# Optimization experiments

Measured on AMD Instinct MI355X. Metric: run time of the kernel, lower is better.

Reference implementation:

```python
import jax, jax.numpy as jnp
import numpy as np

NUM_EMBEDDINGS = 1024
EMBEDDING_DIM = 64
COMMITMENT_COST = 0.25


def setup_inputs() -> dict:
    key = jax.random.key(0)
    k1, k2 = jax.random.split(key)
    inputs = jax.random.normal(k1, (16, EMBEDDING_DIM, 64, 64), dtype=jnp.float32)
    # nn.Embedding weight init: uniform(-1/K, 1/K)
    emb = jax.random.uniform(
        k2, (NUM_EMBEDDINGS, EMBEDDING_DIM), dtype=jnp.float32,
        minval=-1.0 / NUM_EMBEDDINGS, maxval=1.0 / NUM_EMBEDDINGS)
    return {"inputs": inputs, "emb": emb}


def reference(inputs, emb):
    # NCHW -> NHWC
    x = jnp.transpose(inputs, (0, 2, 3, 1))  # [B,H,W,D]
    B, H, W, D = x.shape
    K = emb.shape[0]
    flat = x.reshape(-1, D)  # [N,D]

    # squared L2 distances to every codebook entry: [N,K]
    distances = (jnp.sum(flat * flat, axis=1, keepdims=True)
                 + jnp.sum(emb * emb, axis=1)
                 - 2.0 * jnp.matmul(flat, emb.T))
    idx = jnp.argmin(distances, axis=1)  # [N]
    indices = idx.reshape(B, H, W)[:, None]  # [B,1,H,W]

    # gather == one-hot @ emb, but without the dense matmul
    quantized = emb[idx].reshape(B, H, W, D)

    e_latent_loss = jnp.mean((jax.lax.stop_gradient(quantized) - x) ** 2)
    q_latent_loss = jnp.mean((quantized - jax.lax.stop_gradient(x)) ** 2)
    loss = q_latent_loss + COMMITMENT_COST * e_latent_loss

    # straight-through estimator
    quantized_st = x + jax.lax.stop_gradient(quantized - x)

    # one-hot encodings are part of the module's return contract
    encodings = jax.nn.one_hot(idx, K, dtype=jnp.float32)  # [N,K]
    avg_probs = jnp.mean(encodings, axis=0)
    perplexity = jnp.exp(-jnp.sum(avg_probs * jnp.log(avg_probs + 1e-10)))

    quantized_out = jnp.transpose(quantized_st, (0, 3, 1, 2))  # back to NCHW
    return (loss, quantized_out, perplexity, encodings, indices)
```

## Files before the change

kernel.cpp:

```cpp
#include <hip/hip_runtime.h>

#define NPIX    65536
#define D       64
#define KCODES  1024
#define PIXB    64
#define BLOCK   512
#define XPAD    68
#define XBPAD   72
#define CAP     64
#define GFAC    0.036f

#define QUANT_OFF 1
#define PERP_OFF  4194305
#define ENC_OFF   4194306u
#define IDX_OFF   71303170u


typedef float f32x4 __attribute__((ext_vector_type(4)));
typedef short bf16x8 __attribute__((ext_vector_type(8)));

__device__ __forceinline__ unsigned short f2bf(float f) {
    unsigned u = __float_as_uint(f);
    return (unsigned short)((u + 0x7fffu + ((u >> 16) & 1u)) >> 16);
}

__global__ __launch_bounds__(256) void vq_init(const float* __restrict__ emb,
                                               double* __restrict__ loss_sum,
                                               int* __restrict__ counts,
                                               float* __restrict__ se,
                                               unsigned short* __restrict__ ebf) {
    int t = blockIdx.x * 256 + threadIdx.x;
    if (t == 0) *loss_sum = 0.0;
    if (t < KCODES) {
        counts[t] = 0;
        const float* e = emb + (size_t)t * D;
        float r[8];
        #pragma unroll
        for (int j = 0; j < 8; ++j) r[j] = __fmul_rn(e[j], e[j]);
        #pragma unroll
        for (int i = 8; i < D; i += 8)
            #pragma unroll
            for (int j = 0; j < 8; ++j)
                r[j] = __fadd_rn(r[j], __fmul_rn(e[i + j], e[i + j]));
        float X = __fadd_rn(__fadd_rn(r[0], r[1]), __fadd_rn(r[2], r[3]));
        float Y = __fadd_rn(__fadd_rn(r[4], r[5]), __fadd_rn(r[6], r[7]));
        se[t] = __fadd_rn(X, Y);
        #pragma unroll
        for (int j = 0; j < D; ++j) ebf[(t << 6) + j] = f2bf(e[j]);
    }
}

__global__ __launch_bounds__(512) void vq_main(const float* __restrict__ in,
                                               const float* __restrict__ emb,
                                               const float* __restrict__ se,
                                               const unsigned short* __restrict__ ebf,
                                               float* __restrict__ out,
                                               double* __restrict__ loss_sum,
                                               int* __restrict__ counts) {
    __shared__ float xs[PIXB][XPAD];
    __shared__ unsigned short xb[PIXB][XBPAD];
    __shared__ float sls[KCODES];
    __shared__ float wmin[8][PIXB];
    __shared__ float gate[PIXB];
    __shared__ float sxs[PIXB];
    __shared__ float smx[PIXB];
    __shared__ float semaxsq;
    __shared__ int   cnt[PIXB];
    __shared__ unsigned short list[PIXB][CAP];
    __shared__ int   skfin[PIXB];

    const int tid  = threadIdx.x;
    const int lane = tid & 63;
    const int wid  = tid >> 6;
    const int n0   = blockIdx.x * PIXB;
    const int b    = n0 >> 12;
    const int s0   = n0 & 4095;

    {
        const float* base = in + ((size_t)b << 18) + s0;
        #pragma unroll
        for (int i = 0; i < 8; ++i) {
            int d = wid + (i << 3);
            float v = base[((size_t)d << 12) + lane];
            xs[lane][d] = v;
            xb[lane][d] = f2bf(v);
        }
        sls[tid] = se[tid];
        sls[tid + 512] = se[tid + 512];
    }
    __syncthreads();

    if (tid < PIXB) {
        float r[8];
        #pragma unroll
        for (int j = 0; j < 8; ++j) {
            float v = xs[tid][j];
            r[j] = __fmul_rn(v, v);
        }
        #pragma unroll
        for (int i = 8; i < D; i += 8)
            #pragma unroll
            for (int j = 0; j < 8; ++j) {
                float v = xs[tid][i + j];
                r[j] = __fadd_rn(r[j], __fmul_rn(v, v));
            }
        float X = __fadd_rn(__fadd_rn(r[0], r[1]), __fadd_rn(r[2], r[3]));
        float Y = __fadd_rn(__fadd_rn(r[4], r[5]), __fadd_rn(r[6], r[7]));
        sxs[tid] = __fadd_rn(X, Y);
        float mx = sls[tid << 4];
        #pragma unroll
        for (int j = 1; j < 16; ++j) mx = fmaxf(mx, sls[(tid << 4) + j]);
        smx[tid] = mx;
    }

    const int wbase = wid * 128;
    const int arow  = lane & 15;
    const int kgrp  = (lane >> 4) << 3;
    const int rbase = (lane >> 4) << 2;

    bf16x8 af[2][4];
    #pragma unroll
    for (int ks = 0; ks < 2; ++ks)
        #pragma unroll
        for (int pt = 0; pt < 4; ++pt)
            af[ks][pt] = *(const bf16x8*)&xb[pt * 16 + arow][ks * 32 + kgrp];

    float mreg[4][4];
    #pragma unroll
    for (int pt = 0; pt < 4; ++pt)
        #pragma unroll
        for (int r = 0; r < 4; ++r) mreg[pt][r] = 3.0e38f;

    #pragma unroll
    for (int s = 0; s < 2; ++s) {
        const int cbase = wbase + s * 64;
        f32x4 acc[4][4];
        #pragma unroll
        for (int pt = 0; pt < 4; ++pt)
            #pragma unroll
            for (int kt = 0; kt < 4; ++kt) acc[pt][kt] = (f32x4){0.f, 0.f, 0.f, 0.f};
        #pragma unroll
        for (int ks = 0; ks < 2; ++ks) {
            #pragma unroll
            for (int kt = 0; kt < 4; ++kt) {
                int code = cbase + kt * 16 + arow;
                bf16x8 bf_ = *(const bf16x8*)(ebf + ((size_t)code << 6) + ks * 32 + kgrp);
                #pragma unroll
                for (int pt = 0; pt < 4; ++pt)
                    acc[pt][kt] = __builtin_amdgcn_mfma_f32_16x16x32_bf16(
                        af[ks][pt], bf_, acc[pt][kt], 0, 0, 0);
            }
        }
        #pragma unroll
        for (int pt = 0; pt < 4; ++pt)
            #pragma unroll
            for (int kt = 0; kt < 4; ++kt) {
                int code = cbase + kt * 16 + arow;
                #pragma unroll
                for (int r = 0; r < 4; ++r) {
                    float sv = __fsub_rn(sls[code], __fmul_rn(2.0f, acc[pt][kt][r]));
                    mreg[pt][r] = fminf(mreg[pt][r], sv);
                }
            }
    }
    #pragma unroll
    for (int m = 1; m < 16; m <<= 1)
        #pragma unroll
        for (int pt = 0; pt < 4; ++pt)
            #pragma unroll
            for (int r = 0; r < 4; ++r)
                mreg[pt][r] = fminf(mreg[pt][r], __shfl_xor(mreg[pt][r], m));
    if (arow == 0) {
        #pragma unroll
        for (int pt = 0; pt < 4; ++pt)
            #pragma unroll
            for (int r = 0; r < 4; ++r)
                wmin[wid][pt * 16 + rbase + r] = mreg[pt][r];
    }
    __syncthreads();

    if (tid == 0) {
        float mx = smx[0];
        #pragma unroll
        for (int j = 1; j < PIXB; ++j) mx = fmaxf(mx, smx[j]);
        semaxsq = mx;
    }
    __syncthreads();

    if (tid < PIXB) {
        float gm = wmin[0][tid];
        #pragma unroll
        for (int w = 1; w < 8; ++w) gm = fminf(gm, wmin[w][tid]);
        gate[tid] = gm + GFAC * sqrtf(sxs[tid] * semaxsq);
        cnt[tid] = 0;
    }
    __syncthreads();

    #pragma unroll
    for (int s = 0; s < 2; ++s) {
        const int cbase = wbase + s * 64;
        f32x4 acc[4][4];
        #pragma unroll
        for (int pt = 0; pt < 4; ++pt)
            #pragma unroll
            for (int kt = 0; kt < 4; ++kt) acc[pt][kt] = (f32x4){0.f, 0.f, 0.f, 0.f};
        #pragma unroll
        for (int ks = 0; ks < 2; ++ks) {
            #pragma unroll
            for (int kt = 0; kt < 4; ++kt) {
                int code = cbase + kt * 16 + arow;
                bf16x8 bf_ = *(const bf16x8*)(ebf + ((size_t)code << 6) + ks * 32 + kgrp);
                #pragma unroll
                for (int pt = 0; pt < 4; ++pt)
                    acc[pt][kt] = __builtin_amdgcn_mfma_f32_16x16x32_bf16(
                        af[ks][pt], bf_, acc[pt][kt], 0, 0, 0);
            }
        }
        #pragma unroll
        for (int pt = 0; pt < 4; ++pt)
            #pragma unroll
            for (int kt = 0; kt < 4; ++kt) {
                int code = cbase + kt * 16 + arow;
                #pragma unroll
                for (int r = 0; r < 4; ++r) {
                    float sv = __fsub_rn(sls[code], __fmul_rn(2.0f, acc[pt][kt][r]));
                    int px = pt * 16 + rbase + r;
                    if (sv <= gate[px]) {
                        int slot = atomicAdd(&cnt[px], 1);
                        if (slot < CAP) list[px][slot] = (unsigned short)code;
                    }
                }
            }
    }
    __syncthreads();

    {
        const int px = tid >> 3, c0 = tid & 7;
        const int cn = cnt[px];
        float bv = 3.0e38f;
        int   bk = 0x7fffffff;
        if (cn > CAP) {
            for (int k = c0; k < KCODES; k += 8) {
                const float* er = emb + ((size_t)k << 6);
                float m = 0.f;
                #pragma unroll
                for (int d = 0; d < D; ++d) m = fmaf(xs[px][d], er[d], m);
                float sv = __fsub_rn(__fadd_rn(sxs[px], sls[k]), __fmul_rn(2.0f, m));
                if (sv < bv || (sv == bv && k < bk)) { bv = sv; bk = k; }
            }
        } else {
            for (int i = c0; i < cn; i += 8) {
                int k = list[px][i];
                const float* er = emb + ((size_t)k << 6);
                float m = 0.f;
                #pragma unroll
                for (int d = 0; d < D; ++d) m = fmaf(xs[px][d], er[d], m);
                float sv = __fsub_rn(__fadd_rn(sxs[px], sls[k]), __fmul_rn(2.0f, m));
                if (sv < bv || (sv == bv && k < bk)) { bv = sv; bk = k; }
            }
        }
        #pragma unroll
        for (int m = 4; m; m >>= 1) {
            float ov = __shfl_xor(bv, m);
            int   ok = __shfl_xor(bk, m);
            if (ov < bv || (ov == bv && ok < bk)) { bv = ov; bk = ok; }
        }
        if (c0 == 0) {
            skfin[px] = bk;
            atomicAdd(&counts[bk], 1);
            out[IDX_OFF + (unsigned)(n0 + px)] = (float)bk;
        }
    }
    __syncthreads();

    {
        float* qbase = out + QUANT_OFF + ((size_t)b << 18) + s0;
        float mse = 0.f;
        #pragma unroll
        for (int i = 0; i < 8; ++i) {
            int d = (wid << 3) + i;
            float q = emb[((size_t)skfin[lane] << 6) + d];
            qbase[((size_t)d << 12) + lane] = q;
            float df = q - xs[lane][d];
            mse = fmaf(df, df, mse);
        }
        #pragma unroll
        for (int off = 32; off; off >>= 1) mse += __shfl_down(mse, off);
        if (lane == 0) atomicAdd(loss_sum, (double)mse);
    }

    float4* dst4 = (float4*)(out + ENC_OFF + (size_t)n0 * KCODES + 2);
    for (int i = tid; i < 16383; i += BLOCK) {
        int flat = (i << 2) + 2;
        int r0 = flat >> 10;
        int r1 = (flat + 3) >> 10;
        int k0 = skfin[r0];
        int k1 = skfin[r1];
        int c  = flat & 1023;
        float4 v;
        v.x = (c == k0) ? 1.f : 0.f;
        v.y = (c + 1 == k0) ? 1.f : 0.f;
        v.z = (((flat + 2) & 1023) == k1) ? 1.f : 0.f;
        v.w = (((flat + 3) & 1023) == k1) ? 1.f : 0.f;
        dst4[i] = v;
    }
    if (tid == 0) {
        float2* dh = (float2*)(out + ENC_OFF + (size_t)n0 * KCODES);
        int kh = skfin[0];
        float2 h2; h2.x = (kh == 0) ? 1.f : 0.f; h2.y = (kh == 1) ? 1.f : 0.f;
        *dh = h2;
        float2* dt = (float2*)(out + ENC_OFF + (size_t)n0 * KCODES + 65534);
        int kt = skfin[63];
        float2 t2; t2.x = (kt == 1022) ? 1.f : 0.f; t2.y = (kt == 1023) ? 1.f : 0.f;
        *dt = t2;
    }
}

__global__ __launch_bounds__(256) void vq_fin(const double* __restrict__ loss_sum,
                                              const int* __restrict__ counts,
                                              float* __restrict__ out) {
    __shared__ double red[256];
    int t = threadIdx.x;
    double ent = 0.0;
    for (int k = t; k < KCODES; k += 256) {
        double p = (double)counts[k] / 65536.0;
        ent -= p * log(p + 1e-10);
    }
    red[t] = ent;
    __syncthreads();
    for (int o = 128; o; o >>= 1) {
        if (t < o) red[t] += red[t + o];
        __syncthreads();
    }
    if (t == 0) {
        out[PERP_OFF] = (float)exp(red[0]);
        out[0] = (float)(1.25 * (*loss_sum) / 4194304.0);
    }
}

extern "C" void kernel_launch(void* const* d_in, const int* in_sizes, int n_in,
                              void* d_out, int out_size, void* d_ws, size_t ws_size,
                              hipStream_t stream) {
    const float* in  = (const float*)d_in[0];
    const float* emb = (const float*)d_in[1];
    float* out = (float*)d_out;

    double*         loss_sum = (double*)d_ws;
    int*            counts   = (int*)((char*)d_ws + 8);
    float*          se       = (float*)((char*)d_ws + 4104);
    unsigned short* ebf      = (unsigned short*)((char*)d_ws + 8320);

    vq_init<<<4, 256, 0, stream>>>(emb, loss_sum, counts, se, ebf);
    vq_main<<<NPIX / PIXB, BLOCK, 0, stream>>>(in, emb, se, ebf, out, loss_sum, counts);
    vq_fin<<<1, 256, 0, stream>>>(loss_sum, counts, out);
}
```

Baseline: 185.5 us.

## Split one-hot encoding write into separate kernel and convert A fragments on the fly

```diff
diff --git a/kernel.cpp b/kernel.cpp
--- a/kernel.cpp
+++ b/kernel.cpp
@@ -6,7 +6,6 @@
 #define PIXB    64
 #define BLOCK   512
 #define XPAD    68
-#define XBPAD   72
 #define CAP     64
 #define GFAC    0.036f
 
@@ -58,7 +57,6 @@
                                                double* __restrict__ loss_sum,
                                                int* __restrict__ counts) {
     __shared__ float xs[PIXB][XPAD];
-    __shared__ unsigned short xb[PIXB][XBPAD];
     __shared__ float sls[KCODES];
     __shared__ float wmin[8][PIXB];
     __shared__ float gate[PIXB];
@@ -81,9 +79,7 @@
         #pragma unroll
         for (int i = 0; i < 8; ++i) {
             int d = wid + (i << 3);
-            float v = base[((size_t)d << 12) + lane];
-            xs[lane][d] = v;
-            xb[lane][d] = f2bf(v);
+            xs[lane][d] = base[((size_t)d << 12) + lane];
         }
         sls[tid] = se[tid];
         sls[tid + 512] = se[tid + 512];
@@ -118,13 +114,6 @@
     const int kgrp  = (lane >> 4) << 3;
     const int rbase = (lane >> 4) << 2;
 
-    bf16x8 af[2][4];
-    #pragma unroll
-    for (int ks = 0; ks < 2; ++ks)
-        #pragma unroll
-        for (int pt = 0; pt < 4; ++pt)
-            af[ks][pt] = *(const bf16x8*)&xb[pt * 16 + arow][ks * 32 + kgrp];
-
     float mreg[4][4];
     #pragma unroll
     for (int pt = 0; pt < 4; ++pt)
@@ -141,6 +130,15 @@
             for (int kt = 0; kt < 4; ++kt) acc[pt][kt] = (f32x4){0.f, 0.f, 0.f, 0.f};
         #pragma unroll
         for (int ks = 0; ks < 2; ++ks) {
+            bf16x8 afk[4];
+            #pragma unroll
+            for (int pt = 0; pt < 4; ++pt) {
+                const float* xp = &xs[pt * 16 + arow][ks * 32 + kgrp];
+                bf16x8 v;
+                #pragma unroll
+                for (int j = 0; j < 8; ++j) v[j] = (short)f2bf(xp[j]);
+                afk[pt] = v;
+            }
             #pragma unroll
             for (int kt = 0; kt < 4; ++kt) {
                 int code = cbase + kt * 16 + arow;
@@ -148,7 +146,7 @@
                 #pragma unroll
                 for (int pt = 0; pt < 4; ++pt)
                     acc[pt][kt] = __builtin_amdgcn_mfma_f32_16x16x32_bf16(
-                        af[ks][pt], bf_, acc[pt][kt], 0, 0, 0);
+                        afk[pt], bf_, acc[pt][kt], 0, 0, 0);
             }
         }
         #pragma unroll
@@ -206,6 +204,15 @@
             for (int kt = 0; kt < 4; ++kt) acc[pt][kt] = (f32x4){0.f, 0.f, 0.f, 0.f};
         #pragma unroll
         for (int ks = 0; ks < 2; ++ks) {
+            bf16x8 afk[4];
+            #pragma unroll
+            for (int pt = 0; pt < 4; ++pt) {
+                const float* xp = &xs[pt * 16 + arow][ks * 32 + kgrp];
+                bf16x8 v;
+                #pragma unroll
+                for (int j = 0; j < 8; ++j) v[j] = (short)f2bf(xp[j]);
+                afk[pt] = v;
+            }
             #pragma unroll
             for (int kt = 0; kt < 4; ++kt) {
                 int code = cbase + kt * 16 + arow;
@@ -213,7 +220,7 @@
                 #pragma unroll
                 for (int pt = 0; pt < 4; ++pt)
                     acc[pt][kt] = __builtin_amdgcn_mfma_f32_16x16x32_bf16(
-                        af[ks][pt], bf_, acc[pt][kt], 0, 0, 0);
+                        afk[pt], bf_, acc[pt][kt], 0, 0, 0);
             }
         }
         #pragma unroll
@@ -288,14 +295,22 @@
         for (int off = 32; off; off >>= 1) mse += __shfl_down(mse, off);
         if (lane == 0) atomicAdd(loss_sum, (double)mse);
     }
+}
+
+__global__ __launch_bounds__(512) void vq_enc(float* __restrict__ out) {
+    __shared__ int kf[PIXB];
+    const int tid = threadIdx.x;
+    const int n0  = blockIdx.x * PIXB;
+    if (tid < PIXB) kf[tid] = (int)out[IDX_OFF + (unsigned)(n0 + tid)];
+    __syncthreads();
 
     float4* dst4 = (float4*)(out + ENC_OFF + (size_t)n0 * KCODES + 2);
     for (int i = tid; i < 16383; i += BLOCK) {
         int flat = (i << 2) + 2;
         int r0 = flat >> 10;
         int r1 = (flat + 3) >> 10;
-        int k0 = skfin[r0];
-        int k1 = skfin[r1];
+        int k0 = kf[r0];
+        int k1 = kf[r1];
         int c  = flat & 1023;
         float4 v;
         v.x = (c == k0) ? 1.f : 0.f;
@@ -306,11 +321,11 @@
     }
     if (tid == 0) {
         float2* dh = (float2*)(out + ENC_OFF + (size_t)n0 * KCODES);
-        int kh = skfin[0];
+        int kh = kf[0];
         float2 h2; h2.x = (kh == 0) ? 1.f : 0.f; h2.y = (kh == 1) ? 1.f : 0.f;
         *dh = h2;
         float2* dt = (float2*)(out + ENC_OFF + (size_t)n0 * KCODES + 65534);
-        int kt = skfin[63];
+        int kt = kf[63];
         float2 t2; t2.x = (kt == 1022) ? 1.f : 0.f; t2.y = (kt == 1023) ? 1.f : 0.f;
         *dt = t2;
     }
@@ -352,5 +367,6 @@
 
     vq_init<<<4, 256, 0, stream>>>(emb, loss_sum, counts, se, ebf);
     vq_main<<<NPIX / PIXB, BLOCK, 0, stream>>>(in, emb, se, ebf, out, loss_sum, counts);
+    vq_enc<<<NPIX / PIXB, BLOCK, 0, stream>>>(out);
     vq_fin<<<1, 256, 0, stream>>>(loss_sum, counts, out);
 }
```

New measurement: 197.0 us. 6.2% more time.

## Cut VQ kernel LDS and registers, precompute codebook max, simplify one-hot writes

Applied to the files above, without the earlier changes.

```diff
diff --git a/kernel.cpp b/kernel.cpp
--- a/kernel.cpp
+++ b/kernel.cpp
@@ -6,7 +6,6 @@
 #define PIXB    64
 #define BLOCK   512
 #define XPAD    68
-#define XBPAD   72
 #define CAP     64
 #define GFAC    0.036f
 
@@ -28,6 +27,7 @@
                                                double* __restrict__ loss_sum,
                                                int* __restrict__ counts,
                                                float* __restrict__ se,
+                                               int* __restrict__ semax_bits,
                                                unsigned short* __restrict__ ebf) {
     int t = blockIdx.x * 256 + threadIdx.x;
     if (t == 0) *loss_sum = 0.0;
@@ -44,7 +44,9 @@
                 r[j] = __fadd_rn(r[j], __fmul_rn(e[i + j], e[i + j]));
         float X = __fadd_rn(__fadd_rn(r[0], r[1]), __fadd_rn(r[2], r[3]));
         float Y = __fadd_rn(__fadd_rn(r[4], r[5]), __fadd_rn(r[6], r[7]));
-        se[t] = __fadd_rn(X, Y);
+        float S = __fadd_rn(X, Y);
+        se[t] = S;
+        atomicMax(semax_bits, __float_as_int(S));
         #pragma unroll
         for (int j = 0; j < D; ++j) ebf[(t << 6) + j] = f2bf(e[j]);
     }
@@ -53,21 +55,19 @@
 __global__ __launch_bounds__(512) void vq_main(const float* __restrict__ in,
                                                const float* __restrict__ emb,
                                                const float* __restrict__ se,
+                                               const int* __restrict__ semax_bits,
                                                const unsigned short* __restrict__ ebf,
                                                float* __restrict__ out,
                                                double* __restrict__ loss_sum,
                                                int* __restrict__ counts) {
     __shared__ float xs[PIXB][XPAD];
-    __shared__ unsigned short xb[PIXB][XBPAD];
     __shared__ float sls[KCODES];
     __shared__ float wmin[8][PIXB];
     __shared__ float gate[PIXB];
     __shared__ float sxs[PIXB];
-    __shared__ float smx[PIXB];
-    __shared__ float semaxsq;
     __shared__ int   cnt[PIXB];
+    __shared__ int   skfin[PIXB];
     __shared__ unsigned short list[PIXB][CAP];
-    __shared__ int   skfin[PIXB];
 
     const int tid  = threadIdx.x;
     const int lane = tid & 63;
@@ -81,9 +81,7 @@
         #pragma unroll
         for (int i = 0; i < 8; ++i) {
             int d = wid + (i << 3);
-            float v = base[((size_t)d << 12) + lane];
-            xs[lane][d] = v;
-            xb[lane][d] = f2bf(v);
+            xs[lane][d] = base[((size_t)d << 12) + lane];
         }
         sls[tid] = se[tid];
         sls[tid + 512] = se[tid + 512];
@@ -91,6 +89,7 @@
     __syncthreads();
 
     if (tid < PIXB) {
+        cnt[tid] = 0;
         float r[8];
         #pragma unroll
         for (int j = 0; j < 8; ++j) {
@@ -107,10 +106,6 @@
         float X = __fadd_rn(__fadd_rn(r[0], r[1]), __fadd_rn(r[2], r[3]));
         float Y = __fadd_rn(__fadd_rn(r[4], r[5]), __fadd_rn(r[6], r[7]));
         sxs[tid] = __fadd_rn(X, Y);
-        float mx = sls[tid << 4];
-        #pragma unroll
-        for (int j = 1; j < 16; ++j) mx = fmaxf(mx, sls[(tid << 4) + j]);
-        smx[tid] = mx;
     }
 
     const int wbase = wid * 128;
@@ -122,8 +117,13 @@
     #pragma unroll
     for (int ks = 0; ks < 2; ++ks)
         #pragma unroll
-        for (int pt = 0; pt < 4; ++pt)
-            af[ks][pt] = *(const bf16x8*)&xb[pt * 16 + arow][ks * 32 + kgrp];
+        for (int pt = 0; pt < 4; ++pt) {
+            const float* xp = &xs[pt * 16 + arow][ks * 32 + kgrp];
+            bf16x8 v;
+            #pragma unroll
+            for (int j = 0; j < 8; ++j) v[j] = (short)f2bf(xp[j]);
+            af[ks][pt] = v;
+        }
 
     float mreg[4][4];
     #pragma unroll
@@ -132,17 +132,17 @@
         for (int r = 0; r < 4; ++r) mreg[pt][r] = 3.0e38f;
 
     #pragma unroll
-    for (int s = 0; s < 2; ++s) {
-        const int cbase = wbase + s * 64;
-        f32x4 acc[4][4];
-        #pragma unroll
-        for (int pt = 0; pt < 4; ++pt)
-            #pragma unroll
-            for (int kt = 0; kt < 4; ++kt) acc[pt][kt] = (f32x4){0.f, 0.f, 0.f, 0.f};
-        #pragma unroll
-        for (int ks = 0; ks < 2; ++ks) {
-            #pragma unroll
-            for (int kt = 0; kt < 4; ++kt) {
+    for (int s2 = 0; s2 < 4; ++s2) {
+        const int cbase = wbase + s2 * 32;
+        f32x4 acc[4][2];
+        #pragma unroll
+        for (int pt = 0; pt < 4; ++pt)
+            #pragma unroll
+            for (int kt = 0; kt < 2; ++kt) acc[pt][kt] = (f32x4){0.f, 0.f, 0.f, 0.f};
+        #pragma unroll
+        for (int ks = 0; ks < 2; ++ks)
+            #pragma unroll
+            for (int kt = 0; kt < 2; ++kt) {
                 int code = cbase + kt * 16 + arow;
                 bf16x8 bf_ = *(const bf16x8*)(ebf + ((size_t)code << 6) + ks * 32 + kgrp);
                 #pragma unroll
@@ -150,11 +150,10 @@
                     acc[pt][kt] = __builtin_amdgcn_mfma_f32_16x16x32_bf16(
                         af[ks][pt], bf_, acc[pt][kt], 0, 0, 0);
             }
-        }
-        #pragma unroll
-        for (int pt = 0; pt < 4; ++pt)
-            #pragma unroll
-            for (int kt = 0; kt < 4; ++kt) {
+        #pragma unroll
+        for (int pt = 0; pt < 4; ++pt)
+            #pragma unroll
+            for (int kt = 0; kt < 2; ++kt) {
                 int code = cbase + kt * 16 + arow;
                 #pragma unroll
                 for (int r = 0; r < 4; ++r) {
@@ -179,35 +178,27 @@
     }
     __syncthreads();
 
-    if (tid == 0) {
-        float mx = smx[0];
-        #pragma unroll
-        for (int j = 1; j < PIXB; ++j) mx = fmaxf(mx, smx[j]);
-        semaxsq = mx;
-    }
-    __syncthreads();
-
     if (tid < PIXB) {
         float gm = wmin[0][tid];
         #pragma unroll
         for (int w = 1; w < 8; ++w) gm = fminf(gm, wmin[w][tid]);
-        gate[tid] = gm + GFAC * sqrtf(sxs[tid] * semaxsq);
-        cnt[tid] = 0;
-    }
-    __syncthreads();
-
-    #pragma unroll
-    for (int s = 0; s < 2; ++s) {
-        const int cbase = wbase + s * 64;
-        f32x4 acc[4][4];
-        #pragma unroll
-        for (int pt = 0; pt < 4; ++pt)
-            #pragma unroll
-            for (int kt = 0; kt < 4; ++kt) acc[pt][kt] = (f32x4){0.f, 0.f, 0.f, 0.f};
-        #pragma unroll
-        for (int ks = 0; ks < 2; ++ks) {
-            #pragma unroll
-            for (int kt = 0; kt < 4; ++kt) {
+        float semax = __int_as_float(*semax_bits);
+        gate[tid] = gm + GFAC * sqrtf(sxs[tid] * semax);
+    }
+    __syncthreads();
+
+    #pragma unroll
+    for (int s2 = 0; s2 < 4; ++s2) {
+        const int cbase = wbase + s2 * 32;
+        f32x4 acc[4][2];
+        #pragma unroll
+        for (int pt = 0; pt < 4; ++pt)
+            #pragma unroll
+            for (int kt = 0; kt < 2; ++kt) acc[pt][kt] = (f32x4){0.f, 0.f, 0.f, 0.f};
+        #pragma unroll
+        for (int ks = 0; ks < 2; ++ks)
+            #pragma unroll
+            for (int kt = 0; kt < 2; ++kt) {
                 int code = cbase + kt * 16 + arow;
                 bf16x8 bf_ = *(const bf16x8*)(ebf + ((size_t)code << 6) + ks * 32 + kgrp);
                 #pragma unroll
@@ -215,11 +206,10 @@
                     acc[pt][kt] = __builtin_amdgcn_mfma_f32_16x16x32_bf16(
                         af[ks][pt], bf_, acc[pt][kt], 0, 0, 0);
             }
-        }
-        #pragma unroll
-        for (int pt = 0; pt < 4; ++pt)
-            #pragma unroll
-            for (int kt = 0; kt < 4; ++kt) {
+        #pragma unroll
+        for (int pt = 0; pt < 4; ++pt)
+            #pragma unroll
+            for (int kt = 0; kt < 2; ++kt) {
                 int code = cbase + kt * 16 + arow;
                 #pragma unroll
                 for (int r = 0; r < 4; ++r) {
@@ -239,7 +229,7 @@
         const int cn = cnt[px];
         float bv = 3.0e38f;
         int   bk = 0x7fffffff;
-        if (cn > CAP) {
+        if (cn > CAP || cn == 0) {
             for (int k = c0; k < KCODES; k += 8) {
                 const float* er = emb + ((size_t)k << 6);
                 float m = 0.f;
@@ -289,31 +279,19 @@
         if (lane == 0) atomicAdd(loss_sum, (double)mse);
     }
 
-    float4* dst4 = (float4*)(out + ENC_OFF + (size_t)n0 * KCODES + 2);
-    for (int i = tid; i < 16383; i += BLOCK) {
-        int flat = (i << 2) + 2;
-        int r0 = flat >> 10;
-        int r1 = (flat + 3) >> 10;
-        int k0 = skfin[r0];
-        int k1 = skfin[r1];
-        int c  = flat & 1023;
-        float4 v;
-        v.x = (c == k0) ? 1.f : 0.f;
-        v.y = (c + 1 == k0) ? 1.f : 0.f;
-        v.z = (((flat + 2) & 1023) == k1) ? 1.f : 0.f;
-        v.w = (((flat + 3) & 1023) == k1) ? 1.f : 0.f;
-        dst4[i] = v;
-    }
-    if (tid == 0) {
-        float2* dh = (float2*)(out + ENC_OFF + (size_t)n0 * KCODES);
-        int kh = skfin[0];
-        float2 h2; h2.x = (kh == 0) ? 1.f : 0.f; h2.y = (kh == 1) ? 1.f : 0.f;
-        *dh = h2;
-        float2* dt = (float2*)(out + ENC_OFF + (size_t)n0 * KCODES + 65534);
-        int kt = skfin[63];
-        float2 t2; t2.x = (kt == 1022) ? 1.f : 0.f; t2.y = (kt == 1023) ? 1.f : 0.f;
-        *dt = t2;
-    }
+    {
+        float4* dst4 = (float4*)(out + ENC_OFF + (size_t)n0 * KCODES + 2);
+        const float4 z = {0.f, 0.f, 0.f, 0.f};
+        for (int i = tid; i < 16383; i += BLOCK) dst4[i] = z;
+        if (tid == 0) {
+            const float2 z2 = {0.f, 0.f};
+            *(float2*)(out + ENC_OFF + (size_t)n0 * KCODES) = z2;
+            *(float2*)(out + ENC_OFF + (size_t)n0 * KCODES + 65534) = z2;
+        }
+    }
+    __syncthreads();
+    if (tid < PIXB)
+        out[ENC_OFF + (size_t)(n0 + tid) * KCODES + (unsigned)skfin[tid]] = 1.0f;
 }
 
 __global__ __launch_bounds__(256) void vq_fin(const double* __restrict__ loss_sum,
@@ -345,12 +323,14 @@
     const float* emb = (const float*)d_in[1];
     float* out = (float*)d_out;
 
-    double*         loss_sum = (double*)d_ws;
-    int*            counts   = (int*)((char*)d_ws + 8);
-    float*          se       = (float*)((char*)d_ws + 4104);
-    unsigned short* ebf      = (unsigned short*)((char*)d_ws + 8320);
-
-    vq_init<<<4, 256, 0, stream>>>(emb, loss_sum, counts, se, ebf);
-    vq_main<<<NPIX / PIXB, BLOCK, 0, stream>>>(in, emb, se, ebf, out, loss_sum, counts);
+    double*         loss_sum   = (double*)d_ws;
+    int*            counts     = (int*)((char*)d_ws + 8);
+    float*          se         = (float*)((char*)d_ws + 4104);
+    int*            semax_bits = (int*)((char*)d_ws + 8200);
+    unsigned short* ebf        = (unsigned short*)((char*)d_ws + 8320);
+
+    vq_init<<<4, 256, 0, stream>>>(emb, loss_sum, counts, se, semax_bits, ebf);
+    vq_main<<<NPIX / PIXB, BLOCK, 0, stream>>>(in, emb, se, semax_bits, ebf,
+                                               out, loss_sum, counts);
     vq_fin<<<1, 256, 0, stream>>>(loss_sum, counts, out);
 }
```

New measurement: 164.3 us. 1.13x faster.
